# Optimization experiments

Hardware: AMD Instinct MI355X
Metric: run time of the kernel (lower is better)

## Reference

```python
import jax, jax.numpy as jnp
import numpy as np

B, N, C, H, L, D_FF = 32, 196, 768, 12, 4, 3072

def _ln(x, g, b, eps=1e-6):
    m = x.mean(-1, keepdims=True)
    v = ((x - m) ** 2).mean(-1, keepdims=True)
    return (x - m) / jnp.sqrt(v + eps) * g + b

def _sdpa(q, k, v, scale):
    a = jax.nn.softmax(jnp.einsum('...qd,...kd->...qk', q, k) * scale, axis=-1)
    return jnp.einsum('...qk,...kd->...qd', a, v)

def _vit_attn(x, qkv_w, qkv_b, proj_w, proj_b):
    Bs, Ns, Cs = x.shape
    hd = Cs // H
    qkv = (x @ qkv_w + qkv_b).reshape(Bs, Ns, 3, H, hd).transpose(2, 0, 3, 1, 4)
    q, k, v = qkv[0], qkv[1], qkv[2]  # [B,H,N,hd]
    o = _sdpa(q, k, v, hd ** -0.5).transpose(0, 2, 1, 3).reshape(Bs, Ns, Cs)
    return o @ proj_w + proj_b

def _mlp(x, w1, b1, w2, b2):
    return jax.nn.gelu(x @ w1 + b1, approximate=False) @ w2 + b2

def setup_inputs() -> dict:
    key = jax.random.key(0)
    ks = jax.random.split(key, 16)
    w = lambda k, s: (jax.random.normal(k, s, jnp.float32) * 0.02)
    inp = {
        'x': jax.random.normal(ks[0], (B, N, C), jnp.float32),
        'y': jax.random.normal(ks[1], (B, N, C), jnp.float32),
        'latents': w(ks[2], (1, L, C)),
        'scale_a': jnp.zeros((1,), jnp.float32),
        'scale_v': jnp.zeros((1,), jnp.float32),
    }
    for i, p in enumerate(['s', 'r']):
        kk = jax.random.split(ks[3 + i], 4)
        inp.update({
            f'{p}_ln1_g': jnp.ones((C,), jnp.float32),
            f'{p}_ln1_b': jnp.zeros((C,), jnp.float32),
            f'{p}_qkv_w': w(kk[0], (C, 3 * C)),
            f'{p}_qkv_b': jnp.zeros((3 * C,), jnp.float32),
            f'{p}_proj_w': w(kk[1], (C, C)),
            f'{p}_proj_b': jnp.zeros((C,), jnp.float32),
            f'{p}_ln2_g': jnp.ones((C,), jnp.float32),
            f'{p}_ln2_b': jnp.zeros((C,), jnp.float32),
            f'{p}_fc1_w': w(kk[2], (C, D_FF)),
            f'{p}_fc1_b': jnp.zeros((D_FF,), jnp.float32),
            f'{p}_fc2_w': w(kk[3], (D_FF, C)),
            f'{p}_fc2_b': jnp.zeros((C,), jnp.float32),
        })
    return inp

def reference(x, y, latents, scale_a, scale_v,
              s_ln1_g, s_ln1_b, s_qkv_w, s_qkv_b, s_proj_w, s_proj_b,
              s_ln2_g, s_ln2_b, s_fc1_w, s_fc1_b, s_fc2_w, s_fc2_b,
              r_ln1_g, r_ln1_b, r_qkv_w, r_qkv_b, r_proj_w, r_proj_b,
              r_ln2_g, r_ln2_b, r_fc1_w, r_fc1_b, r_fc2_w, r_fc2_b):
    BS = x.shape[0]
    Cf = x.shape[-1]
    # --- latent bottleneck fusion (single-head, scale = C**-0.5) ---
    concat = jnp.concatenate([x, y], axis=1)            # [B, Na+Nv, C]
    lat = jnp.broadcast_to(latents, (BS,) + latents.shape[1:])
    fused = _sdpa(lat, concat, concat, Cf ** -0.5)      # [B, L, C]
    x = x + scale_a * _sdpa(x, fused, fused, Cf ** -0.5)
    y = y + scale_v * _sdpa(y, fused, fused, Cf ** -0.5)
    # --- standard ViT blocks per stream ---
    x = x + _vit_attn(_ln(x, s_ln1_g, s_ln1_b), s_qkv_w, s_qkv_b, s_proj_w, s_proj_b)
    y = y + _vit_attn(_ln(y, r_ln1_g, r_ln1_b), r_qkv_w, r_qkv_b, r_proj_w, r_proj_b)
    x = x + _mlp(_ln(x, s_ln2_g, s_ln2_b), s_fc1_w, s_fc1_b, s_fc2_w, s_fc2_b)
    y = y + _mlp(_ln(y, r_ln2_g, r_ln2_b), r_fc1_w, r_fc1_b, r_fc2_w, r_fc2_b)
    return (x, y)
```

## Files before the change

### kernel.cpp

```cpp
#include <hip/hip_runtime.h>
#include <hip/hip_bf16.h>
#include <math.h>

constexpr int Bc   = 32;
constexpr int Nc   = 196;
constexpr int Cc   = 768;
constexpr int Hc   = 12;
constexpr int HDc  = 64;
constexpr int Lc   = 4;
constexpr int DFFc = 3072;
constexpr int NCAT = 2 * Nc;
constexpr int Mrows = Bc * Nc;
constexpr float SCALE_C = 0.03608439182435161f;
constexpr float SCALE_H = 0.125f;
constexpr float LOG2E   = 1.4426950408889634f;

typedef __attribute__((ext_vector_type(8))) short short8;
typedef __attribute__((ext_vector_type(4))) short s16x4;
typedef __attribute__((ext_vector_type(4))) float float4a;
typedef __attribute__((ext_vector_type(4))) _Float16 half4;

__device__ inline float gelu_fast(float v) {
    float c = v * (0.7978845608028654f + 0.035677408136300125f * v * v);
    float ex = __expf(2.f * c);
    float th = 1.f - 2.f / (ex + 1.f);
    return 0.5f * v * (1.f + th);
}

__device__ inline void store_val(float* p, float v) { *p = v; }
__device__ inline void store_val(__hip_bfloat16* p, float v) { *p = __float2bfloat16(v); }

__device__ inline void gload16(const void* g, void* l) {
    __builtin_amdgcn_global_load_lds(
        (const __attribute__((address_space(1))) void*)g,
        (__attribute__((address_space(3))) void*)l, 16, 0, 0);
}

__global__ __launch_bounds__(256) void lat_scores_ker(
    const float* __restrict__ x, const float* __restrict__ y,
    const float* __restrict__ lat, float* __restrict__ scores)
{
    int wglobal = blockIdx.x * 4 + (threadIdx.x >> 6);
    int lane = threadIdx.x & 63;
    int b = wglobal / NCAT, j = wglobal % NCAT;
    const float* row = (j < Nc) ? x + ((size_t)b * Nc + j) * Cc
                                : y + ((size_t)b * Nc + (j - Nc)) * Cc;
    float a0 = 0.f, a1 = 0.f, a2 = 0.f, a3 = 0.f;
    for (int c = lane; c < Cc; c += 64) {
        float rv = row[c];
        a0 += rv * lat[c];
        a1 += rv * lat[Cc + c];
        a2 += rv * lat[2 * Cc + c];
        a3 += rv * lat[3 * Cc + c];
    }
    #pragma unroll
    for (int o = 32; o; o >>= 1) {
        a0 += __shfl_xor(a0, o);
        a1 += __shfl_xor(a1, o);
        a2 += __shfl_xor(a2, o);
        a3 += __shfl_xor(a3, o);
    }
    if (lane == 0) {
        float* sb = scores + (size_t)b * Lc * NCAT + j;
        sb[0 * NCAT] = a0 * SCALE_C;
        sb[1 * NCAT] = a1 * SCALE_C;
        sb[2 * NCAT] = a2 * SCALE_C;
        sb[3 * NCAT] = a3 * SCALE_C;
    }
}

__global__ __launch_bounds__(256) void lat_softmax_ker(float* __restrict__ scores)
{
    int b = blockIdx.x;
    int w = threadIdx.x >> 6, lane = threadIdx.x & 63;
    float* row = scores + (size_t)b * Lc * NCAT + w * NCAT;
    float m = -INFINITY;
    for (int j = lane; j < NCAT; j += 64) m = fmaxf(m, row[j]);
    #pragma unroll
    for (int o = 32; o; o >>= 1) m = fmaxf(m, __shfl_xor(m, o));
    float sum = 0.f;
    float e0 = expf(row[lane] - m);
    float e1 = expf(row[lane + 64] - m);
    float e2 = expf(row[lane + 128] - m);
    float e3 = expf(row[lane + 192] - m);
    float e4 = expf(row[lane + 256] - m);
    float e5 = expf(row[lane + 320] - m);
    float e6 = (lane < 8) ? expf(row[lane + 384] - m) : 0.f;
    sum = e0 + e1 + e2 + e3 + e4 + e5 + e6;
    #pragma unroll
    for (int o = 32; o; o >>= 1) sum += __shfl_xor(sum, o);
    float inv = 1.f / sum;
    row[lane] = e0 * inv;
    row[lane + 64] = e1 * inv;
    row[lane + 128] = e2 * inv;
    row[lane + 192] = e3 * inv;
    row[lane + 256] = e4 * inv;
    row[lane + 320] = e5 * inv;
    if (lane < 8) row[lane + 384] = e6 * inv;
}

__global__ __launch_bounds__(256) void lat_fused_ker(
    const float* __restrict__ x, const float* __restrict__ y,
    const float* __restrict__ probs, float* __restrict__ fused)
{
    int b = blockIdx.x, chunk = blockIdx.y;
    int t = threadIdx.x;
    int l = t >> 6;
    int c = chunk * 64 + (t & 63);
    __shared__ float p[Lc][NCAT];
    for (int idx = t; idx < Lc * NCAT; idx += 256)
        (&p[0][0])[idx] = probs[(size_t)b * Lc * NCAT + idx];
    __syncthreads();

    float acc0 = 0.f, acc1 = 0.f;
    for (int j = 0; j < Nc; j += 2) {
        const float* r0 = x + ((size_t)b * Nc + j) * Cc;
        acc0 += p[l][j] * r0[c];
        acc1 += p[l][j + 1] * r0[Cc + c];
    }
    for (int j = 0; j < Nc; j += 2) {
        const float* r0 = y + ((size_t)b * Nc + j) * Cc;
        acc0 += p[l][Nc + j] * r0[c];
        acc1 += p[l][Nc + j + 1] * r0[Cc + c];
    }
    fused[(size_t)b * Lc * Cc + l * Cc + c] = acc0 + acc1;
}

__global__ __launch_bounds__(256) void inject_ker(
    const float* __restrict__ x, const float* __restrict__ y,
    const float* __restrict__ fused,
    const float* __restrict__ scale_a, const float* __restrict__ scale_v,
    float* __restrict__ out)
{
    int gid = blockIdx.x;
    int st = gid / Mrows;
    int bn = gid % Mrows;
    int b = bn / Nc;
    const float* src = st ? y : x;
    float scale = st ? scale_v[0] : scale_a[0];
    float* dst = out + (size_t)st * Mrows * Cc;
    const float* f = fused + (size_t)b * Lc * Cc;
    const float* row = src + (size_t)bn * Cc;

    __shared__ float sc[4];
    int w = threadIdx.x >> 6, lane = threadIdx.x & 63;
    float partial = 0.f;
    for (int c = lane; c < Cc; c += 64) partial += row[c] * f[w * Cc + c];
    #pragma unroll
    for (int o = 32; o; o >>= 1) partial += __shfl_xor(partial, o);
    if (lane == 0) sc[w] = partial * SCALE_C;
    __syncthreads();

    float s0 = sc[0], s1 = sc[1], s2 = sc[2], s3 = sc[3];
    float m = fmaxf(fmaxf(s0, s1), fmaxf(s2, s3));
    float e0 = expf(s0 - m), e1 = expf(s1 - m), e2 = expf(s2 - m), e3 = expf(s3 - m);
    float inv = 1.f / (e0 + e1 + e2 + e3);
    e0 *= inv; e1 *= inv; e2 *= inv; e3 *= inv;

    for (int c = threadIdx.x; c < Cc; c += 256) {
        float v = e0 * f[c] + e1 * f[Cc + c] + e2 * f[2 * Cc + c] + e3 * f[3 * Cc + c];
        dst[(size_t)bn * Cc + c] = row[c] + scale * v;
    }
}

__global__ __launch_bounds__(256) void inject_ln_ker(
    const float* __restrict__ x, const float* __restrict__ y,
    const float* __restrict__ fusedb,
    const float* __restrict__ scale_a, const float* __restrict__ scale_v,
    const float* __restrict__ ga, const float* __restrict__ ba,
    const float* __restrict__ gv, const float* __restrict__ bv,
    float* __restrict__ out, __hip_bfloat16* __restrict__ lnout, size_t lnz)
{
    int gid = blockIdx.x;
    int st = gid / Mrows;
    int bn = gid % Mrows;
    int b = bn / Nc;
    const float* src = st ? y : x;
    float scale = st ? scale_v[0] : scale_a[0];
    const float* g  = st ? gv : ga;
    const float* bb = st ? bv : ba;
    float* dst = out + (size_t)st * Mrows * Cc + (size_t)bn * Cc;
    __hip_bfloat16* lno = lnout + (size_t)st * lnz + (size_t)bn * Cc;
    const float* f = fusedb + (size_t)b * Lc * Cc;
    const float* row = src + (size_t)bn * Cc;

    __shared__ float sc[4];
    __shared__ float red[4];
    int t = threadIdx.x;
    int w = t >> 6, lane = t & 63;
    float partial = 0.f;
    for (int c = lane; c < Cc; c += 64) partial += row[c] * f[w * Cc + c];
    #pragma unroll
    for (int o = 32; o; o >>= 1) partial += __shfl_xor(partial, o);
    if (lane == 0) sc[w] = partial * SCALE_C;
    __syncthreads();

    float s0 = sc[0], s1 = sc[1], s2 = sc[2], s3 = sc[3];
    float m = fmaxf(fmaxf(s0, s1), fmaxf(s2, s3));
    float e0 = expf(s0 - m), e1 = expf(s1 - m), e2 = expf(s2 - m), e3 = expf(s3 - m);
    float inv = 1.f / (e0 + e1 + e2 + e3);
    e0 *= inv; e1 *= inv; e2 *= inv; e3 *= inv;

    float u[3];
    float s = 0.f;
    #pragma unroll
    for (int k = 0; k < 3; ++k) {
        int c = t + 256 * k;
        float v = e0 * f[c] + e1 * f[Cc + c] + e2 * f[2 * Cc + c] + e3 * f[3 * Cc + c];
        u[k] = row[c] + scale * v;
        s += u[k];
    }
    #pragma unroll
    for (int o = 32; o; o >>= 1) s += __shfl_xor(s, o);
    if (lane == 0) red[w] = s;
    __syncthreads();
    float mean = (red[0] + red[1] + red[2] + red[3]) * (1.f / Cc);

    float vs = 0.f;
    #pragma unroll
    for (int k = 0; k < 3; ++k) { float d = u[k] - mean; vs += d * d; }
    #pragma unroll
    for (int o = 32; o; o >>= 1) vs += __shfl_xor(vs, o);
    __syncthreads();
    if (lane == 0) red[w] = vs;
    __syncthreads();
    float var = (red[0] + red[1] + red[2] + red[3]) * (1.f / Cc);
    float rinv = 1.f / sqrtf(var + 1e-6f);

    #pragma unroll
    for (int k = 0; k < 3; ++k) {
        int c = t + 256 * k;
        dst[c] = u[k];
        lno[c] = __float2bfloat16((u[k] - mean) * rinv * g[c] + bb[c]);
    }
}

__global__ __launch_bounds__(256) void ln_ker(
    const float* __restrict__ in, size_t inz,
    const float* __restrict__ g0, const float* __restrict__ b0,
    const float* __restrict__ g1, const float* __restrict__ b1,
    __hip_bfloat16* __restrict__ out, size_t outz)
{
    int z = blockIdx.z;
    const float* g = z ? g1 : g0;
    const float* bb = z ? b1 : b0;
    in += (size_t)z * inz; out += (size_t)z * outz;

    int row = blockIdx.x;
    __shared__ float buf[Cc];
    __shared__ float red[4];
    __shared__ float red2[4];
    const float* r = in + (size_t)row * Cc;
    int w = threadIdx.x >> 6, lane = threadIdx.x & 63;

    float s = 0.f;
    for (int c = threadIdx.x; c < Cc; c += 256) {
        float v = r[c];
        buf[c] = v;
        s += v;
    }
    #pragma unroll
    for (int o = 32; o; o >>= 1) s += __shfl_xor(s, o);
    if (lane == 0) red[w] = s;
    __syncthreads();
    float mean = (red[0] + red[1] + red[2] + red[3]) * (1.f / Cc);

    float vs = 0.f;
    for (int c = threadIdx.x; c < Cc; c += 256) {
        float d = buf[c] - mean;
        vs += d * d;
    }
    #pragma unroll
    for (int o = 32; o; o >>= 1) vs += __shfl_xor(vs, o);
    if (lane == 0) red2[w] = vs;
    __syncthreads();
    float var = (red2[0] + red2[1] + red2[2] + red2[3]) * (1.f / Cc);
    float inv = 1.f / sqrtf(var + 1e-6f);

    for (int c = threadIdx.x; c < Cc; c += 256)
        out[(size_t)row * Cc + c] =
            __float2bfloat16((buf[c] - mean) * inv * g[c] + bb[c]);
}

struct WArgs {
    const float* src[8];
    __hip_bfloat16* dst[8];
};

__global__ __launch_bounds__(256) void wcast_all_ker(WArgs wa)
{
    int z = blockIdx.z;
    int bx = blockIdx.x;
    int which, tile, K_, N_;
    if (bx < 1728)      { which = 0; tile = bx;        K_ = 768;  N_ = 2304; }
    else if (bx < 2304) { which = 1; tile = bx - 1728; K_ = 768;  N_ = 768;  }
    else if (bx < 4608) { which = 2; tile = bx - 2304; K_ = 768;  N_ = 3072; }
    else                { which = 3; tile = bx - 4608; K_ = 3072; N_ = 768;  }
    const float* W = wa.src[z * 4 + which];
    __hip_bfloat16* WT = wa.dst[z * 4 + which];
    int ntx = N_ >> 5;
    int n0 = (tile % ntx) * 32, k0 = (tile / ntx) * 32;

    __shared__ float tilebuf[32][33];
    int t = threadIdx.x;
    int r = t >> 5, c = t & 31;
    #pragma unroll
    for (int p = 0; p < 4; ++p)
        tilebuf[r + p * 8][c] = W[(size_t)(k0 + r + p * 8) * N_ + n0 + c];
    __syncthreads();
    #pragma unroll
    for (int p = 0; p < 4; ++p)
        WT[(size_t)(n0 + r + p * 8) * K_ + k0 + c] =
            __float2bfloat16(tilebuf[c][r + p * 8]);
}

template <int EPI, typename OutT>
__global__ __launch_bounds__(256, 4) void gemm_bf16_ker(
    const __hip_bfloat16* __restrict__ A, size_t Az,
    const __hip_bfloat16* __restrict__ BT, size_t BTz,
    const float* __restrict__ bias0, const float* __restrict__ bias1,
    const float* __restrict__ res, size_t resz,
    OutT* __restrict__ out, size_t outz,
    int M_, int N_, int K_)
{
    const int gx = gridDim.x, gy = gridDim.y;
    const long T = (long)gx * gy * gridDim.z;
    long iflat = blockIdx.x + (long)gx * (blockIdx.y + (long)gy * blockIdx.z);
    long q = T >> 3, r = T & 7;
    long xcd = iflat & 7, jj = iflat >> 3;
    long tt = (xcd < r ? xcd * (q + 1) : r * (q + 1) + (xcd - r) * q) + jj;
    const int bx = (int)(tt % gx);
    const int by = (int)((tt / gx) % gy);
    const int z  = (int)(tt / ((long)gx * gy));

    A += (size_t)z * Az;
    BT += (size_t)z * BTz;
    const float* bias = z ? bias1 : bias0;
    res += (size_t)z * resz;
    out += (size_t)z * outz;

    __shared__ short As[128 * 64];
    __shared__ short Bs[128 * 64];
    const int t = threadIdx.x;
    const int wid = t >> 6, lane = t & 63;
    const int row0 = by * 128, col0 = bx * 128;
    const int wr = (wid >> 1) * 64, wc = (wid & 1) * 64;

    const __hip_bfloat16* aSrc[4];
    const __hip_bfloat16* bSrc[4];
    int ldsOff[4];
    #pragma unroll
    for (int ii = 0; ii < 4; ++ii) {
        int f = wid * 1024 + ii * 4096 + lane * 16;
        int rw = f >> 7;
        int us = ((f >> 4) & 7) ^ (rw & 7);
        aSrc[ii] = A + (size_t)(row0 + rw) * K_ + us * 8;
        bSrc[ii] = BT + (size_t)(col0 + rw) * K_ + us * 8;
        ldsOff[ii] = (wid * 1024 + ii * 4096) >> 1;
    }

    const int fr = lane & 15;
    const int ku = lane >> 4;
    int rlA[4], rlB[4];
    #pragma unroll
    for (int m = 0; m < 4; ++m) {
        rlA[m] = wr + m * 16 + fr;
        rlB[m] = wc + m * 16 + fr;
    }

    float4a acc[4][4];
    #pragma unroll
    for (int m = 0; m < 4; ++m)
        #pragma unroll
        for (int n = 0; n < 4; ++n)
            acc[m][n] = (float4a)0.f;

    for (int kt = 0; kt < K_; kt += 64) {
        #pragma unroll
        for (int ii = 0; ii < 4; ++ii) {
            gload16(aSrc[ii] + kt, As + ldsOff[ii]);
            gload16(bSrc[ii] + kt, Bs + ldsOff[ii]);
        }
        __syncthreads();

        #pragma unroll
        for (int s = 0; s < 2; ++s) {
            short8 af[4], bf8[4];
            #pragma unroll
            for (int m = 0; m < 4; ++m) {
                int u = (s * 4 + ku) ^ (rlA[m] & 7);
                af[m] = *(const short8*)(As + rlA[m] * 64 + u * 8);
            }
            #pragma unroll
            for (int n = 0; n < 4; ++n) {
                int u = (s * 4 + ku) ^ (rlB[n] & 7);
                bf8[n] = *(const short8*)(Bs + rlB[n] * 64 + u * 8);
            }
            #pragma unroll
            for (int m = 0; m < 4; ++m)
                #pragma unroll
                for (int n = 0; n < 4; ++n)
                    acc[m][n] = __builtin_amdgcn_mfma_f32_16x16x32_bf16(
                        af[m], bf8[n], acc[m][n], 0, 0, 0);
        }
        __syncthreads();
    }

    const int fq = lane >> 4;
    #pragma unroll
    for (int m = 0; m < 4; ++m) {
        #pragma unroll
        for (int n = 0; n < 4; ++n) {
            int col = col0 + wc + n * 16 + fr;
            float b = bias[col];
            #pragma unroll
            for (int j = 0; j < 4; ++j) {
                int row = row0 + wr + m * 16 + fq * 4 + j;
                float v = acc[m][n][j] + b;
                if (EPI == 1) v = gelu_fast(v);
                if (EPI == 2) v += res[(size_t)row * N_ + col];
                store_val(out + (size_t)row * N_ + col, v);
            }
        }
    }
}

constexpr int NKT = 13;
constexpr int NQT = 13;
constexpr int NPAD = NKT * 16;
constexpr int VTS = 216;

__global__ __launch_bounds__(256) void attn_mfma_ker(
    const __hip_bfloat16* __restrict__ qkv, size_t qz,
    __hip_bfloat16* __restrict__ o, size_t oz)
{
    int z = blockIdx.z;
    qkv += (size_t)z * qz;
    o += (size_t)z * oz;

    int h = blockIdx.x, b = blockIdx.y;
    __shared__ short Ks[NPAD * 64];
    __shared__ _Float16 VT[64 * VTS];
    const size_t rs = 3 * Cc;
    const __hip_bfloat16* base = qkv + (size_t)b * Nc * rs + h * HDc;
    const int t = threadIdx.x;

    for (int c = t; c < NPAD * 8; c += 256) {
        int row = c >> 3, u = c & 7;
        int srow = row < Nc ? row : Nc - 1;
        short8 kv = *(const short8*)(base + (size_t)srow * rs + Cc + u * 8);
        *(short8*)(Ks + row * 64 + ((u ^ (row & 7)) << 3)) = kv;
        short8 vv = *(const short8*)(base + (size_t)srow * rs + 2 * Cc + u * 8);
        #pragma unroll
        for (int w = 0; w < 8; ++w) {
            __hip_bfloat16 bvv = ((const __hip_bfloat16*)&vv)[w];
            VT[(u * 8 + w) * VTS + row] = (_Float16)__bfloat162float(bvv);
        }
    }
    __syncthreads();

    const int wv = t >> 6, lane = t & 63;
    const int g = lane >> 4, c16 = lane & 15;
    const float KS = SCALE_H * LOG2E;

    for (int qt = wv; qt < NQT; qt += 4) {
        int qrow = qt * 16 + c16;
        int sq = qrow < Nc ? qrow : Nc - 1;
        const __hip_bfloat16* qb = base + (size_t)sq * rs + g * 8;
        short8 bq0 = *(const short8*)(qb);
        short8 bq1 = *(const short8*)(qb + 32);

        float4a acc[NKT];
        #pragma unroll
        for (int kt = 0; kt < NKT; ++kt) acc[kt] = (float4a)0.f;
        #pragma unroll
        for (int kt = 0; kt < NKT; ++kt) {
            int r = kt * 16 + c16;
            short8 a0 = *(const short8*)(Ks + r * 64 + ((g ^ (r & 7)) << 3));
            short8 a1 = *(const short8*)(Ks + r * 64 + (((4 + g) ^ (r & 7)) << 3));
            acc[kt] = __builtin_amdgcn_mfma_f32_16x16x32_bf16(a0, bq0, acc[kt], 0, 0, 0);
            acc[kt] = __builtin_amdgcn_mfma_f32_16x16x32_bf16(a1, bq1, acc[kt], 0, 0, 0);
        }

        float m = -INFINITY;
        #pragma unroll
        for (int kt = 0; kt < NKT; ++kt) {
            #pragma unroll
            for (int j = 0; j < 4; ++j) {
                int key = kt * 16 + g * 4 + j;
                float v = (key < Nc) ? acc[kt][j] * KS : -INFINITY;
                acc[kt][j] = v;
                m = fmaxf(m, v);
            }
        }
        m = fmaxf(m, __shfl_xor(m, 16));
        m = fmaxf(m, __shfl_xor(m, 32));

        float sum = 0.f;
        half4 pb[NKT];
        #pragma unroll
        for (int kt = 0; kt < NKT; ++kt) {
            #pragma unroll
            for (int j = 0; j < 4; ++j) {
                float e = exp2f(acc[kt][j] - m);
                sum += e;
                pb[kt][j] = (_Float16)e;
            }
        }
        sum += __shfl_xor(sum, 16);
        sum += __shfl_xor(sum, 32);
        float inv = 1.f / sum;

        float4a oa[4];
        #pragma unroll
        for (int dt = 0; dt < 4; ++dt) oa[dt] = (float4a)0.f;
        #pragma unroll
        for (int kt = 0; kt < NKT; ++kt) {
            #pragma unroll
            for (int dt = 0; dt < 4; ++dt) {
                half4 av = *(const half4*)(VT + (size_t)(dt * 16 + c16) * VTS
                                              + kt * 16 + g * 4);
                oa[dt] = __builtin_amdgcn_mfma_f32_16x16x16f16(av, pb[kt], oa[dt], 0, 0, 0);
            }
        }

        if (qrow < Nc) {
            __hip_bfloat16* ob = o + ((size_t)b * Nc + qrow) * Cc + h * HDc;
            #pragma unroll
            for (int dt = 0; dt < 4; ++dt) {
                __hip_bfloat16 tmp[4];
                #pragma unroll
                for (int j = 0; j < 4; ++j)
                    tmp[j] = __float2bfloat16(oa[dt][j] * inv);
                *(s16x4*)(ob + dt * 16 + g * 4) = *(const s16x4*)tmp;
            }
        }
    }
}

extern "C" void kernel_launch(void* const* d_in, const int* in_sizes, int n_in,
                              void* d_out, int out_size, void* d_ws, size_t ws_size,
                              hipStream_t stream)
{
    const float* x       = (const float*)d_in[0];
    const float* y       = (const float*)d_in[1];
    const float* latents = (const float*)d_in[2];
    const float* scale_a = (const float*)d_in[3];
    const float* scale_v = (const float*)d_in[4];

    float* out = (float*)d_out;

    constexpr size_t WSTREAM = 7077888;
    constexpr size_t OFF_QKV = 0;
    constexpr size_t OFF_PROJ = 2304 * 768;
    constexpr size_t OFF_FC1 = OFF_PROJ + 768 * 768;
    constexpr size_t OFF_FC2 = OFF_FC1 + 3072 * 768;

    constexpr size_t FRONT = ((size_t)Bc * Lc * NCAT + (size_t)Bc * Lc * Cc) * 4;
    constexpr size_t NEED_BATCH = FRONT
        + 2 * (size_t)Mrows * Cc * 2
        + 2 * (size_t)Mrows * DFFc * 2
        + 2 * WSTREAM * 2;

    float* ws = (float*)d_ws;
    float* scores = ws;
    float* fusedb = scores + (size_t)Bc * Lc * NCAT;

    const bool batched = ws_size >= NEED_BATCH;

    __hip_bfloat16* tbuf = (__hip_bfloat16*)(fusedb + (size_t)Bc * Lc * Cc);
    __hip_bfloat16* big;
    __hip_bfloat16* wT;
    if (batched) {
        big = tbuf + 2 * (size_t)Mrows * Cc;
        wT  = big + 2 * (size_t)Mrows * DFFc;
    } else {
        big = tbuf + (size_t)Mrows * Cc;
        wT  = big + (size_t)Mrows * DFFc;
    }

    lat_scores_ker<<<Bc * NCAT / 4, 256, 0, stream>>>(x, y, latents, scores);
    lat_softmax_ker<<<Bc, 256, 0, stream>>>(scores);
    lat_fused_ker<<<dim3(Bc, 12), 256, 0, stream>>>(x, y, scores, fusedb);

    WArgs wa;
    for (int p = 0; p < 2; ++p) {
        int basei = 5 + 12 * p;
        wa.src[p * 4 + 0] = (const float*)d_in[basei + 2];
        wa.src[p * 4 + 1] = (const float*)d_in[basei + 4];
        wa.src[p * 4 + 2] = (const float*)d_in[basei + 8];
        wa.src[p * 4 + 3] = (const float*)d_in[basei + 10];
        wa.dst[p * 4 + 0] = wT + p * WSTREAM + OFF_QKV;
        wa.dst[p * 4 + 1] = wT + p * WSTREAM + OFF_PROJ;
        wa.dst[p * 4 + 2] = wT + p * WSTREAM + OFF_FC1;
        wa.dst[p * 4 + 3] = wT + p * WSTREAM + OFF_FC2;
    }

    const float* g1[2], *b1[2], *qkvb[2], *projb[2], *g2[2], *b2[2], *fc1b[2], *fc2b[2];
    for (int p = 0; p < 2; ++p) {
        int basei = 5 + 12 * p;
        g1[p]    = (const float*)d_in[basei + 0];
        b1[p]    = (const float*)d_in[basei + 1];
        qkvb[p]  = (const float*)d_in[basei + 3];
        projb[p] = (const float*)d_in[basei + 5];
        g2[p]    = (const float*)d_in[basei + 6];
        b2[p]    = (const float*)d_in[basei + 7];
        fc1b[p]  = (const float*)d_in[basei + 9];
        fc2b[p]  = (const float*)d_in[basei + 11];
    }

    const size_t MC = (size_t)Mrows * Cc;
    const size_t MQKV = (size_t)Mrows * 2304;
    const size_t MFF = (size_t)Mrows * DFFc;

    if (batched) {
        inject_ln_ker<<<2 * Mrows, 256, 0, stream>>>(
            x, y, fusedb, scale_a, scale_v,
            g1[0], b1[0], g1[1], b1[1], out, tbuf, MC);
        wcast_all_ker<<<dim3(6912, 1, 2), 256, 0, stream>>>(wa);
        gemm_bf16_ker<0, __hip_bfloat16><<<dim3(18, 49, 2), 256, 0, stream>>>(
            tbuf, MC, wT + OFF_QKV, WSTREAM, qkvb[0], qkvb[1],
            (const float*)out, 0, big, MQKV, Mrows, 2304, 768);
        attn_mfma_ker<<<dim3(Hc, Bc, 2), 256, 0, stream>>>(big, MQKV, tbuf, MC);
        gemm_bf16_ker<2, float><<<dim3(6, 49, 2), 256, 0, stream>>>(
            tbuf, MC, wT + OFF_PROJ, WSTREAM, projb[0], projb[1],
            (const float*)out, MC, out, MC, Mrows, 768, 768);
        ln_ker<<<dim3(Mrows, 1, 2), 256, 0, stream>>>(
            out, MC, g2[0], b2[0], g2[1], b2[1], tbuf, MC);
        gemm_bf16_ker<1, __hip_bfloat16><<<dim3(24, 49, 2), 256, 0, stream>>>(
            tbuf, MC, wT + OFF_FC1, WSTREAM, fc1b[0], fc1b[1],
            (const float*)out, 0, big, MFF, Mrows, 3072, 768);
        gemm_bf16_ker<2, float><<<dim3(6, 49, 2), 256, 0, stream>>>(
            big, MFF, wT + OFF_FC2, WSTREAM, fc2b[0], fc2b[1],
            (const float*)out, MC, out, MC, Mrows, 768, 3072);
    } else {
        inject_ker<<<2 * Mrows, 256, 0, stream>>>(x, y, fusedb, scale_a, scale_v, out);
        wcast_all_ker<<<dim3(6912, 1, 2), 256, 0, stream>>>(wa);
        for (int p = 0; p < 2; ++p) {
            float* X = out + (size_t)p * MC;
            __hip_bfloat16* wb = wT + p * WSTREAM;
            ln_ker<<<dim3(Mrows, 1, 1), 256, 0, stream>>>(
                X, 0, g1[p], b1[p], g1[p], b1[p], tbuf, 0);
            gemm_bf16_ker<0, __hip_bfloat16><<<dim3(18, 49, 1), 256, 0, stream>>>(
                tbuf, 0, wb + OFF_QKV, 0, qkvb[p], qkvb[p],
                (const float*)X, 0, big, 0, Mrows, 2304, 768);
            attn_mfma_ker<<<dim3(Hc, Bc, 1), 256, 0, stream>>>(big, 0, tbuf, 0);
            gemm_bf16_ker<2, float><<<dim3(6, 49, 1), 256, 0, stream>>>(
                tbuf, 0, wb + OFF_PROJ, 0, projb[p], projb[p],
                (const float*)X, 0, X, 0, Mrows, 768, 768);
            ln_ker<<<dim3(Mrows, 1, 1), 256, 0, stream>>>(
                X, 0, g2[p], b2[p], g2[p], b2[p], tbuf, 0);
            gemm_bf16_ker<1, __hip_bfloat16><<<dim3(24, 49, 1), 256, 0, stream>>>(
                tbuf, 0, wb + OFF_FC1, 0, fc1b[p], fc1b[p],
                (const float*)X, 0, big, 0, Mrows, 3072, 768);
            gemm_bf16_ker<2, float><<<dim3(6, 49, 1), 256, 0, stream>>>(
                big, 0, wb + OFF_FC2, 0, fc2b[p], fc2b[p],
                (const float*)X, 0, X, 0, Mrows, 768, 3072);
        }
    }
}
```

Before: 410.8 us.

## Fuse latent softmax into fused kernel and overlap GEMM tile loads with MFMA

Drops the separate latent softmax kernel and recomputes the softmax in shared memory inside each lat_fused block, saving one launch and a global round trip. The bf16 GEMM main loop now reads the whole K-tile's fragments from LDS into registers, syncs, starts the next tile's global-to-LDS loads, and then runs the MFMAs, so load latency can hide behind compute. This doubles the fragment registers held per thread, which may lower occupancy. Each of the 12 column chunks repeats the softmax redundantly.

```diff
diff --git a/kernel.cpp b/kernel.cpp
--- a/kernel.cpp
+++ b/kernel.cpp
@@ -69,49 +69,37 @@
     }
 }
 
-__global__ __launch_bounds__(256) void lat_softmax_ker(float* __restrict__ scores)
-{
-    int b = blockIdx.x;
-    int w = threadIdx.x >> 6, lane = threadIdx.x & 63;
-    float* row = scores + (size_t)b * Lc * NCAT + w * NCAT;
-    float m = -INFINITY;
-    for (int j = lane; j < NCAT; j += 64) m = fmaxf(m, row[j]);
-    #pragma unroll
-    for (int o = 32; o; o >>= 1) m = fmaxf(m, __shfl_xor(m, o));
-    float sum = 0.f;
-    float e0 = expf(row[lane] - m);
-    float e1 = expf(row[lane + 64] - m);
-    float e2 = expf(row[lane + 128] - m);
-    float e3 = expf(row[lane + 192] - m);
-    float e4 = expf(row[lane + 256] - m);
-    float e5 = expf(row[lane + 320] - m);
-    float e6 = (lane < 8) ? expf(row[lane + 384] - m) : 0.f;
-    sum = e0 + e1 + e2 + e3 + e4 + e5 + e6;
-    #pragma unroll
-    for (int o = 32; o; o >>= 1) sum += __shfl_xor(sum, o);
-    float inv = 1.f / sum;
-    row[lane] = e0 * inv;
-    row[lane + 64] = e1 * inv;
-    row[lane + 128] = e2 * inv;
-    row[lane + 192] = e3 * inv;
-    row[lane + 256] = e4 * inv;
-    row[lane + 320] = e5 * inv;
-    if (lane < 8) row[lane + 384] = e6 * inv;
-}
-
 __global__ __launch_bounds__(256) void lat_fused_ker(
     const float* __restrict__ x, const float* __restrict__ y,
-    const float* __restrict__ probs, float* __restrict__ fused)
+    const float* __restrict__ scores, float* __restrict__ fused)
 {
     int b = blockIdx.x, chunk = blockIdx.y;
     int t = threadIdx.x;
-    int l = t >> 6;
-    int c = chunk * 64 + (t & 63);
     __shared__ float p[Lc][NCAT];
     for (int idx = t; idx < Lc * NCAT; idx += 256)
-        (&p[0][0])[idx] = probs[(size_t)b * Lc * NCAT + idx];
-    __syncthreads();
-
+        (&p[0][0])[idx] = scores[(size_t)b * Lc * NCAT + idx];
+    __syncthreads();
+    int w = t >> 6, lane = t & 63;
+    {
+        float m = -INFINITY;
+        for (int j = lane; j < NCAT; j += 64) m = fmaxf(m, p[w][j]);
+        #pragma unroll
+        for (int o = 32; o; o >>= 1) m = fmaxf(m, __shfl_xor(m, o));
+        float sum = 0.f;
+        for (int j = lane; j < NCAT; j += 64) {
+            float e = expf(p[w][j] - m);
+            p[w][j] = e;
+            sum += e;
+        }
+        #pragma unroll
+        for (int o = 32; o; o >>= 1) sum += __shfl_xor(sum, o);
+        float inv = 1.f / sum;
+        for (int j = lane; j < NCAT; j += 64) p[w][j] *= inv;
+    }
+    __syncthreads();
+
+    int l = w;
+    int c = chunk * 64 + lane;
     float acc0 = 0.f, acc1 = 0.f;
     for (int j = 0; j < Nc; j += 2) {
         const float* r0 = x + ((size_t)b * Nc + j) * Cc;
@@ -375,36 +363,49 @@
         for (int n = 0; n < 4; ++n)
             acc[m][n] = (float4a)0.f;
 
+#define STAGE(KT)                                                     \
+    {                                                                 \
+        _Pragma("unroll")                                             \
+        for (int ii = 0; ii < 4; ++ii) {                              \
+            gload16(aSrc[ii] + (KT), As + ldsOff[ii]);                \
+            gload16(bSrc[ii] + (KT), Bs + ldsOff[ii]);                \
+        }                                                             \
+    }
+
+    STAGE(0);
+    __syncthreads();
+
     for (int kt = 0; kt < K_; kt += 64) {
-        #pragma unroll
-        for (int ii = 0; ii < 4; ++ii) {
-            gload16(aSrc[ii] + kt, As + ldsOff[ii]);
-            gload16(bSrc[ii] + kt, Bs + ldsOff[ii]);
-        }
-        __syncthreads();
-
+        short8 af[2][4], bf8[2][4];
         #pragma unroll
         for (int s = 0; s < 2; ++s) {
-            short8 af[4], bf8[4];
             #pragma unroll
             for (int m = 0; m < 4; ++m) {
                 int u = (s * 4 + ku) ^ (rlA[m] & 7);
-                af[m] = *(const short8*)(As + rlA[m] * 64 + u * 8);
+                af[s][m] = *(const short8*)(As + rlA[m] * 64 + u * 8);
             }
             #pragma unroll
             for (int n = 0; n < 4; ++n) {
                 int u = (s * 4 + ku) ^ (rlB[n] & 7);
-                bf8[n] = *(const short8*)(Bs + rlB[n] * 64 + u * 8);
+                bf8[s][n] = *(const short8*)(Bs + rlB[n] * 64 + u * 8);
             }
+        }
+        __syncthreads();
+
+        if (kt + 64 < K_) STAGE(kt + 64);
+
+        #pragma unroll
+        for (int s = 0; s < 2; ++s)
             #pragma unroll
             for (int m = 0; m < 4; ++m)
                 #pragma unroll
                 for (int n = 0; n < 4; ++n)
                     acc[m][n] = __builtin_amdgcn_mfma_f32_16x16x32_bf16(
-                        af[m], bf8[n], acc[m][n], 0, 0, 0);
-        }
+                        af[s][m], bf8[s][n], acc[m][n], 0, 0, 0);
+
         __syncthreads();
     }
+#undef STAGE
 
     const int fq = lane >> 4;
     #pragma unroll
@@ -580,7 +581,6 @@
     }
 
     lat_scores_ker<<<Bc * NCAT / 4, 256, 0, stream>>>(x, y, latents, scores);
-    lat_softmax_ker<<<Bc, 256, 0, stream>>>(scores);
     lat_fused_ker<<<dim3(Bc, 12), 256, 0, stream>>>(x, y, scores, fusedb);
 
     WArgs wa;
```

Result: slower. 905.3 us (median of 2 runs) (+120.4%).
